# Optimization experiments

Measured on AMD Instinct MI355X. Metric: run time of the kernel, lower is better.

## Reference

```python
import jax, jax.numpy as jnp
import numpy as np

POS_DIM = 3
LATENT = 128
HEADS = 4
HEAD_DIM = LATENT // HEADS
KERNEL_IN = 4 * POS_DIM - POS_DIM + 1  # q_pos,o_pos,rel,dist -> 10
N_Q = 1024
N_O = 2048
LN_EPS = 1e-5


def setup_inputs() -> dict:
    key = jax.random.key(0)
    ks = jax.random.split(key, 9)
    s = lambda fan_in: 1.0 / np.sqrt(fan_in)
    return {
        "h_obs": jax.random.normal(ks[0], (N_O, LATENT), dtype=jnp.float32),
        "pos_obs": jax.random.normal(ks[1], (N_O, POS_DIM), dtype=jnp.float32),
        "pos_query": jax.random.normal(ks[2], (N_Q, POS_DIM), dtype=jnp.float32),
        "obs_batch": jnp.zeros((N_O,), dtype=jnp.int32),
        "query_batch": jnp.zeros((N_Q,), dtype=jnp.int32),
        # kernel_mlp: Linear(10, 128) -> ReLU -> Linear(128, 4); stored as [in, out]
        "W1": jax.random.uniform(ks[3], (KERNEL_IN, LATENT), jnp.float32, -s(KERNEL_IN), s(KERNEL_IN)),
        "b1": jnp.zeros((LATENT,), jnp.float32),
        "W2": jax.random.uniform(ks[4], (LATENT, HEADS), jnp.float32, -s(LATENT), s(LATENT)),
        "b2": jnp.zeros((HEADS,), jnp.float32),
        "ln_gamma": jnp.ones((LATENT,), jnp.float32),
        "ln_beta": jnp.zeros((LATENT,), jnp.float32),
        "Wv": jax.random.uniform(ks[5], (LATENT, LATENT), jnp.float32, -s(LATENT), s(LATENT)),
        "bv": jnp.zeros((LATENT,), jnp.float32),
    }


def reference(h_obs, pos_obs, pos_query, obs_batch, query_batch,
              W1, b1, W2, b2, ln_gamma, ln_beta, Wv, bv):
    N_q, N_o = pos_query.shape[0], pos_obs.shape[0]
    # pairwise relative position encodings: [N_q, N_o, 10]
    rel = pos_query[:, None, :] - pos_obs[None, :, :]            # [N_q, N_o, P]
    dist = jnp.linalg.norm(rel, axis=-1, keepdims=True)          # [N_q, N_o, 1]
    pos_q_exp = jnp.broadcast_to(pos_query[:, None, :], rel.shape)
    pos_o_exp = jnp.broadcast_to(pos_obs[None, :, :], rel.shape)
    kernel_input = jnp.concatenate([pos_q_exp, pos_o_exp, rel, dist], axis=-1)
    # per-pair MLP score -> logits [N_q, N_o, H]
    hidden = jax.nn.relu(jnp.einsum('qok,kl->qol', kernel_input, W1) + b1)
    logits = jnp.einsum('qol,lh->qoh', hidden, W2) + b2
    # same-graph mask (softmax over N_o axis)
    batch_mask = query_batch[:, None] == obs_batch[None, :]      # [N_q, N_o]
    logits = jnp.where(batch_mask[:, :, None], logits, -jnp.inf)
    weights = jax.nn.softmax(logits, axis=1)                     # over N_o
    # value path: LayerNorm -> value_proj -> heads
    mu = jnp.mean(h_obs, axis=-1, keepdims=True)
    var = jnp.var(h_obs, axis=-1, keepdims=True)
    h_norm = (h_obs - mu) * jax.lax.rsqrt(var + LN_EPS) * ln_gamma + ln_beta
    v = (h_norm @ Wv + bv).reshape(N_o, HEADS, HEAD_DIM)         # [N_o, H, D]
    # weighted aggregation: [N_q, H, D] -> [N_q, latent]
    h_query = jnp.einsum('qoh,ohd->qhd', weights, v)
    return h_query.reshape(N_q, LATENT)
```

## Files before the change

kernel.cpp:

```cpp
#include <hip/hip_runtime.h>

#define NQ 1024
#define NO 2048
#define LAT 128
#define CHUNK 16
#define NCHUNK (NO / CHUNK)
#define LDSTR 132
#define LOG2E 1.4426950408889634f
#define NEG_BIG -3.0e38f
#define MASK_THRESH -1.0e37f
#define PART_STRIDE 136
#define SY_MAX 32

__global__ __launch_bounds__(256) void gano_value(
    const float* __restrict__ ln_g,
    const float* __restrict__ ln_b,
    const float* __restrict__ Wv,
    const float* __restrict__ bv,
    float* __restrict__ h)
{
    __shared__ float hn[2][LAT];
    __shared__ float red[2][4];
    const int t = threadIdx.x;
    const int o = t >> 7;
    const int d = t & 127;
    const int ob = blockIdx.x * 2 + o;

    const float x = h[(size_t)ob*LAT + d];
    float s1 = x, s2 = x*x;
#pragma unroll
    for (int off = 32; off >= 1; off >>= 1) {
        s1 += __shfl_xor(s1, off);
        s2 += __shfl_xor(s2, off);
    }
    const int wv = (t >> 6) & 1;
    if ((t & 63) == 0) { red[o][wv*2] = s1; red[o][wv*2+1] = s2; }
    __syncthreads();
    const float S1 = red[o][0] + red[o][2];
    const float S2 = red[o][1] + red[o][3];
    const float mean = S1 * (1.0f/LAT);
    const float var  = S2 * (1.0f/LAT) - mean*mean;
    const float rstd = rsqrtf(var + 1e-5f);
    hn[o][d] = (x - mean) * rstd * ln_g[d] + ln_b[d];
    __syncthreads();

    float a0 = bv[d], a1 = 0.f, a2 = 0.f, a3 = 0.f;
    const float* wc = Wv + d;
    const float* hh = hn[o];
#pragma unroll 8
    for (int kk = 0; kk < 32; ++kk) {
        a0 = fmaf(hh[kk],      wc[(size_t)(kk)*LAT],      a0);
        a1 = fmaf(hh[kk + 32], wc[(size_t)(kk + 32)*LAT], a1);
        a2 = fmaf(hh[kk + 64], wc[(size_t)(kk + 64)*LAT], a2);
        a3 = fmaf(hh[kk + 96], wc[(size_t)(kk + 96)*LAT], a3);
    }
    h[(size_t)ob*LAT + d] = (a0 + a1) + (a2 + a3);
}

__global__ __launch_bounds__(256) void gano_main(
    const float* __restrict__ v,
    const float* __restrict__ pos_obs,
    const float* __restrict__ pos_query,
    const int* __restrict__ obs_batch,
    const int* __restrict__ query_batch,
    const float* __restrict__ W1,
    const float* __restrict__ b1,
    const float* __restrict__ W2,
    const float* __restrict__ b2,
    float* __restrict__ ws,
    float* __restrict__ out,
    int SY)
{
    __shared__ __align__(16) float ld[CHUNK*LDSTR];
    __shared__ __align__(16) float lcq[16*LDSTR];
    __shared__ __align__(16) float lgt[16*4*CHUNK];
    __shared__ float lpos[CHUNK*3];
    __shared__ int   lob[CHUNK];

    const int tid = threadIdx.x;
    const int i  = tid & 15;
    const int qi = tid >> 4;
    const int q  = blockIdx.x * 16 + qi;
    const int d0 = i * 8;
    const int hstar = i >> 2;

#pragma unroll
    for (int t2 = 0; t2 < 2; ++t2) {
        const int idx = tid + t2*256;
        const int row = idx >> 5;
        const int g   = idx & 31;
        const int dd4 = g * 4;
        const int qq  = blockIdx.x * 16 + row;
        const float px = pos_query[qq*3+0];
        const float py = pos_query[qq*3+1];
        const float pz = pos_query[qq*3+2];
        float4 c = *(const float4*)(b1 + dd4);
        const float4 wx0 = *(const float4*)(W1 + 0*LAT + dd4);
        const float4 wx6 = *(const float4*)(W1 + 6*LAT + dd4);
        const float4 wy0 = *(const float4*)(W1 + 1*LAT + dd4);
        const float4 wy6 = *(const float4*)(W1 + 7*LAT + dd4);
        const float4 wz0 = *(const float4*)(W1 + 2*LAT + dd4);
        const float4 wz6 = *(const float4*)(W1 + 8*LAT + dd4);
        c.x = fmaf(px, wx0.x+wx6.x, fmaf(py, wy0.x+wy6.x, fmaf(pz, wz0.x+wz6.x, c.x)));
        c.y = fmaf(px, wx0.y+wx6.y, fmaf(py, wy0.y+wy6.y, fmaf(pz, wz0.y+wz6.y, c.y)));
        c.z = fmaf(px, wx0.z+wx6.z, fmaf(py, wy0.z+wy6.z, fmaf(pz, wz0.z+wz6.z, c.z)));
        c.w = fmaf(px, wx0.w+wx6.w, fmaf(py, wy0.w+wy6.w, fmaf(pz, wz0.w+wz6.w, c.w)));
        *(float4*)(lcq + row*LDSTR + dd4) = c;
    }

    const float pqx = pos_query[q*3+0];
    const float pqy = pos_query[q*3+1];
    const float pqz = pos_query[q*3+2];
    const int   qb  = query_batch[q];
    const float b2l0 = b2[0]*LOG2E, b2l1 = b2[1]*LOG2E;
    const float b2l2 = b2[2]*LOG2E, b2l3 = b2[3]*LOG2E;

    float4 accA = make_float4(0.f,0.f,0.f,0.f);
    float4 accB = make_float4(0.f,0.f,0.f,0.f);
    float m = NEG_BIG, lsum = 0.f;

    for (int cb = blockIdx.y; cb < NCHUNK; cb += SY) {
        const int o0 = cb * CHUNK;
        __syncthreads();

#pragma unroll
        for (int t2 = 0; t2 < 2; ++t2) {
            const int idx = tid + t2*256;
            const int oo = idx >> 5;
            const int g  = idx & 31;
            const int d4 = g * 4;
            const float* po = pos_obs + (size_t)(o0 + oo)*3;
            const float px = po[0], py = po[1], pz = po[2];
            const float4 w3 = *(const float4*)(W1 + 3*LAT + d4);
            const float4 w4 = *(const float4*)(W1 + 4*LAT + d4);
            const float4 w5 = *(const float4*)(W1 + 5*LAT + d4);
            const float4 w6 = *(const float4*)(W1 + 6*LAT + d4);
            const float4 w7 = *(const float4*)(W1 + 7*LAT + d4);
            const float4 w8 = *(const float4*)(W1 + 8*LAT + d4);
            float4 r;
            r.x = fmaf(px, w3.x-w6.x, fmaf(py, w4.x-w7.x, pz*(w5.x-w8.x)));
            r.y = fmaf(px, w3.y-w6.y, fmaf(py, w4.y-w7.y, pz*(w5.y-w8.y)));
            r.z = fmaf(px, w3.z-w6.z, fmaf(py, w4.z-w7.z, pz*(w5.z-w8.z)));
            r.w = fmaf(px, w3.w-w6.w, fmaf(py, w4.w-w7.w, pz*(w5.w-w8.w)));
            *(float4*)(ld + oo*LDSTR + d4) = r;
        }
        for (int idx = tid; idx < CHUNK*3; idx += 256) lpos[idx] = pos_obs[o0*3 + idx];
        for (int idx = tid; idx < CHUNK;   idx += 256) lob[idx]  = obs_batch[o0 + idx];
        __syncthreads();

        {
            const int oc = i;
            const float dx = pqx - lpos[oc*3+0];
            const float dy = pqy - lpos[oc*3+1];
            const float dz = pqz - lpos[oc*3+2];
            const float dist = sqrtf(dx*dx + dy*dy + dz*dz);
            const int mb = (lob[oc] == qb);

            float lg0 = 0.f, lg1 = 0.f, lg2 = 0.f, lg3 = 0.f;
            const float* ldr = ld + oc*LDSTR;
            const float* lcr = lcq + qi*LDSTR;
#pragma unroll 4
            for (int j = 0; j < 32; ++j) {
                const float4 dd = *(const float4*)(ldr + j*4);
                const float4 cc = *(const float4*)(lcr + j*4);
                const float4 wd = *(const float4*)(W1 + 9*LAT + j*4);
                const float4 w2a = *(const float4*)(W2 + (j*4+0)*4);
                const float4 w2b = *(const float4*)(W2 + (j*4+1)*4);
                const float4 w2c = *(const float4*)(W2 + (j*4+2)*4);
                const float4 w2d = *(const float4*)(W2 + (j*4+3)*4);
                const float h0 = fmaxf(fmaf(wd.x, dist, cc.x + dd.x), 0.f);
                const float h1 = fmaxf(fmaf(wd.y, dist, cc.y + dd.y), 0.f);
                const float h2 = fmaxf(fmaf(wd.z, dist, cc.z + dd.z), 0.f);
                const float h3 = fmaxf(fmaf(wd.w, dist, cc.w + dd.w), 0.f);
                lg0 = fmaf(h0, w2a.x, lg0); lg1 = fmaf(h0, w2a.y, lg1);
                lg2 = fmaf(h0, w2a.z, lg2); lg3 = fmaf(h0, w2a.w, lg3);
                lg0 = fmaf(h1, w2b.x, lg0); lg1 = fmaf(h1, w2b.y, lg1);
                lg2 = fmaf(h1, w2b.z, lg2); lg3 = fmaf(h1, w2b.w, lg3);
                lg0 = fmaf(h2, w2c.x, lg0); lg1 = fmaf(h2, w2c.y, lg1);
                lg2 = fmaf(h2, w2c.z, lg2); lg3 = fmaf(h2, w2c.w, lg3);
                lg0 = fmaf(h3, w2d.x, lg0); lg1 = fmaf(h3, w2d.y, lg1);
                lg2 = fmaf(h3, w2d.z, lg2); lg3 = fmaf(h3, w2d.w, lg3);
            }
            const int ocr = (oc + 4*qi) & 15;
            float* lrow = lgt + (qi*4)*CHUNK + ocr;
            lrow[0*CHUNK] = mb ? fmaf(lg0, LOG2E, b2l0) : NEG_BIG;
            lrow[1*CHUNK] = mb ? fmaf(lg1, LOG2E, b2l1) : NEG_BIG;
            lrow[2*CHUNK] = mb ? fmaf(lg2, LOG2E, b2l2) : NEG_BIG;
            lrow[3*CHUNK] = mb ? fmaf(lg3, LOG2E, b2l3) : NEG_BIG;
        }
        __syncthreads();

        {
            const float* rowp = lgt + (qi*4 + hstar)*CHUNK;
#pragma unroll
            for (int og = 0; og < 4; ++og) {
                const float4 t4 = *(const float4*)(rowp + ((og + qi) & 3) * 4);
#pragma unroll
                for (int pr = 0; pr < 2; ++pr) {
                    const float l0 = pr ? t4.z : t4.x;
                    const float l1 = pr ? t4.w : t4.y;
                    const float mn = fmaxf(m, fmaxf(l0, l1));
                    const float alpha = exp2f(m - mn);
                    const float p0 = (l0 > MASK_THRESH) ? exp2f(l0 - mn) : 0.f;
                    const float p1 = (l1 > MASK_THRESH) ? exp2f(l1 - mn) : 0.f;
                    lsum = fmaf(lsum, alpha, p0 + p1);
                    m = mn;

                    const float* vp = v + (size_t)(o0 + og*4 + pr*2)*LAT + d0;
                    const float4 v0A = *(const float4*)(vp);
                    const float4 v0B = *(const float4*)(vp + 4);
                    const float4 v1A = *(const float4*)(vp + LAT);
                    const float4 v1B = *(const float4*)(vp + LAT + 4);
                    accA.x = fmaf(accA.x, alpha, fmaf(p0, v0A.x, p1*v1A.x));
                    accA.y = fmaf(accA.y, alpha, fmaf(p0, v0A.y, p1*v1A.y));
                    accA.z = fmaf(accA.z, alpha, fmaf(p0, v0A.z, p1*v1A.z));
                    accA.w = fmaf(accA.w, alpha, fmaf(p0, v0A.w, p1*v1A.w));
                    accB.x = fmaf(accB.x, alpha, fmaf(p0, v0B.x, p1*v1B.x));
                    accB.y = fmaf(accB.y, alpha, fmaf(p0, v0B.y, p1*v1B.y));
                    accB.z = fmaf(accB.z, alpha, fmaf(p0, v0B.z, p1*v1B.z));
                    accB.w = fmaf(accB.w, alpha, fmaf(p0, v0B.w, p1*v1B.w));
                }
            }
        }
    }

    if (SY == 1) {
        const float inv = 1.0f / lsum;
        float* op = out + (size_t)q*LAT + d0;
        float4 rA, rB;
        rA.x = accA.x*inv; rA.y = accA.y*inv; rA.z = accA.z*inv; rA.w = accA.w*inv;
        rB.x = accB.x*inv; rB.y = accB.y*inv; rB.z = accB.z*inv; rB.w = accB.w*inv;
        *(float4*)op       = rA;
        *(float4*)(op + 4) = rB;
    } else {
        float* pp = ws + ((size_t)blockIdx.y * NQ + q) * PART_STRIDE;
        if ((i & 3) == 0) {
            pp[hstar]     = m;
            pp[4 + hstar] = lsum;
        }
        *(float4*)(pp + 8 + d0)     = accA;
        *(float4*)(pp + 8 + d0 + 4) = accB;
    }
}

__global__ __launch_bounds__(128) void gano_combine(
    const float* __restrict__ ws, float* __restrict__ out, int SY)
{
    __shared__ float lm[SY_MAX*4];
    __shared__ float ll[SY_MAX*4];
    const int q = blockIdx.x;
    const int l = threadIdx.x;
    const int h = l >> 5;

    if (l < SY*4) {
        const int s = l >> 2, hh = l & 3;
        const float* pp = ws + ((size_t)s * NQ + q) * PART_STRIDE;
        lm[l] = pp[hh];
        ll[l] = pp[4 + hh];
    }
    __syncthreads();

    float M = NEG_BIG;
    for (int s = 0; s < SY; ++s) M = fmaxf(M, lm[s*4 + h]);

    float Ls = 0.f, A0 = 0.f, A1 = 0.f;
#pragma unroll 4
    for (int s = 0; s + 1 < SY; s += 2) {
        const float e0 = exp2f(lm[s*4 + h] - M);
        const float e1 = exp2f(lm[(s+1)*4 + h] - M);
        Ls = fmaf(ll[s*4 + h], e0, fmaf(ll[(s+1)*4 + h], e1, Ls));
        A0 = fmaf(ws[((size_t)s     * NQ + q) * PART_STRIDE + 8 + l], e0, A0);
        A1 = fmaf(ws[((size_t)(s+1) * NQ + q) * PART_STRIDE + 8 + l], e1, A1);
    }
    if (SY & 1) {
        const int s = SY - 1;
        const float e0 = exp2f(lm[s*4 + h] - M);
        Ls = fmaf(ll[s*4 + h], e0, Ls);
        A0 = fmaf(ws[((size_t)s * NQ + q) * PART_STRIDE + 8 + l], e0, A0);
    }
    out[(size_t)q*LAT + l] = (A0 + A1) / Ls;
}

extern "C" void kernel_launch(void* const* d_in, const int* in_sizes, int n_in,
                              void* d_out, int out_size, void* d_ws, size_t ws_size,
                              hipStream_t stream) {
    (void)in_sizes; (void)n_in; (void)out_size;
    float*       h_obs     = (float*)d_in[0];
    const float* pos_obs   = (const float*)d_in[1];
    const float* pos_query = (const float*)d_in[2];
    const int*   obs_batch = (const int*)d_in[3];
    const int*   query_batch = (const int*)d_in[4];
    const float* W1 = (const float*)d_in[5];
    const float* b1 = (const float*)d_in[6];
    const float* W2 = (const float*)d_in[7];
    const float* b2 = (const float*)d_in[8];
    const float* ln_g = (const float*)d_in[9];
    const float* ln_b = (const float*)d_in[10];
    const float* Wv = (const float*)d_in[11];
    const float* bv = (const float*)d_in[12];
    float* ws  = (float*)d_ws;
    float* out = (float*)d_out;

    int SY = 1;
    const size_t per = (size_t)NQ * PART_STRIDE * sizeof(float);
    if (ws && ws_size >= 2*per) {
        size_t s = ws_size / per;
        SY = (int)(s < SY_MAX ? s : SY_MAX);
    }

    gano_value<<<NO/2, 256, 0, stream>>>(ln_g, ln_b, Wv, bv, h_obs);
    gano_main<<<dim3(NQ/16, SY), 256, 0, stream>>>(h_obs, pos_obs, pos_query,
                                                   obs_batch, query_batch,
                                                   W1, b1, W2, b2, ws, out, SY);
    if (SY > 1)
        gano_combine<<<NQ, 128, 0, stream>>>(ws, out, SY);
}
```

Measured before the change: 191.6 us.

## Precompute per-observation W1 terms globally and fuse split-K combine via last-block atomic

Per-observation first-layer contributions are now computed once in the value kernel and stored in workspace, instead of being rebuilt into shared memory for every chunk by every query block. The main loop reads them from global memory, which removes the staging stores and one barrier per chunk. The separate combine kernel is removed: the last block for each query tile, found through an atomic counter, merges the partial softmax results. This saves a launch and a pass over the workspace, at the cost of extra global traffic in the inner loop and threadfence/atomic overhead.

```diff
diff --git a/kernel.cpp b/kernel.cpp
--- a/kernel.cpp
+++ b/kernel.cpp
@@ -12,12 +12,19 @@
 #define PART_STRIDE 136
 #define SY_MAX 32
 
+#define WS_DO   0
+#define WS_CNT  (NO*LAT)
+#define WS_PART (NO*LAT + 64)
+
 __global__ __launch_bounds__(256) void gano_value(
     const float* __restrict__ ln_g,
     const float* __restrict__ ln_b,
     const float* __restrict__ Wv,
     const float* __restrict__ bv,
-    float* __restrict__ h)
+    const float* __restrict__ W1,
+    const float* __restrict__ pos_obs,
+    float* __restrict__ h,
+    float* __restrict__ wsf)
 {
     __shared__ float hn[2][LAT];
     __shared__ float red[2][4];
@@ -35,6 +42,17 @@
     }
     const int wv = (t >> 6) & 1;
     if ((t & 63) == 0) { red[o][wv*2] = s1; red[o][wv*2+1] = s2; }
+
+    if (wsf) {
+        const float p0 = pos_obs[ob*3+0];
+        const float p1 = pos_obs[ob*3+1];
+        const float p2 = pos_obs[ob*3+2];
+        float ds =      p0 * (W1[3*LAT + d] - W1[6*LAT + d]);
+        ds = fmaf(p1,        W1[4*LAT + d] - W1[7*LAT + d], ds);
+        ds = fmaf(p2,        W1[5*LAT + d] - W1[8*LAT + d], ds);
+        wsf[WS_DO + (size_t)ob*LAT + d] = ds;
+        if (blockIdx.x == 0 && t < 64) ((int*)(wsf + WS_CNT))[t] = 0;
+    }
     __syncthreads();
     const float S1 = red[o][0] + red[o][2];
     const float S2 = red[o][1] + red[o][3];
@@ -71,11 +89,9 @@
     float* __restrict__ out,
     int SY)
 {
-    __shared__ __align__(16) float ld[CHUNK*LDSTR];
     __shared__ __align__(16) float lcq[16*LDSTR];
     __shared__ __align__(16) float lgt[16*4*CHUNK];
-    __shared__ float lpos[CHUNK*3];
-    __shared__ int   lob[CHUNK];
+    __shared__ int lastflag;
 
     const int tid = threadIdx.x;
     const int i  = tid & 15;
@@ -119,69 +135,83 @@
     float4 accB = make_float4(0.f,0.f,0.f,0.f);
     float m = NEG_BIG, lsum = 0.f;
 
+    const float* dob = ws ? (ws + WS_DO) : nullptr;
+
     for (int cb = blockIdx.y; cb < NCHUNK; cb += SY) {
         const int o0 = cb * CHUNK;
         __syncthreads();
 
-#pragma unroll
-        for (int t2 = 0; t2 < 2; ++t2) {
-            const int idx = tid + t2*256;
-            const int oo = idx >> 5;
-            const int g  = idx & 31;
-            const int d4 = g * 4;
-            const float* po = pos_obs + (size_t)(o0 + oo)*3;
-            const float px = po[0], py = po[1], pz = po[2];
-            const float4 w3 = *(const float4*)(W1 + 3*LAT + d4);
-            const float4 w4 = *(const float4*)(W1 + 4*LAT + d4);
-            const float4 w5 = *(const float4*)(W1 + 5*LAT + d4);
-            const float4 w6 = *(const float4*)(W1 + 6*LAT + d4);
-            const float4 w7 = *(const float4*)(W1 + 7*LAT + d4);
-            const float4 w8 = *(const float4*)(W1 + 8*LAT + d4);
-            float4 r;
-            r.x = fmaf(px, w3.x-w6.x, fmaf(py, w4.x-w7.x, pz*(w5.x-w8.x)));
-            r.y = fmaf(px, w3.y-w6.y, fmaf(py, w4.y-w7.y, pz*(w5.y-w8.y)));
-            r.z = fmaf(px, w3.z-w6.z, fmaf(py, w4.z-w7.z, pz*(w5.z-w8.z)));
-            r.w = fmaf(px, w3.w-w6.w, fmaf(py, w4.w-w7.w, pz*(w5.w-w8.w)));
-            *(float4*)(ld + oo*LDSTR + d4) = r;
-        }
-        for (int idx = tid; idx < CHUNK*3; idx += 256) lpos[idx] = pos_obs[o0*3 + idx];
-        for (int idx = tid; idx < CHUNK;   idx += 256) lob[idx]  = obs_batch[o0 + idx];
-        __syncthreads();
-
         {
-            const int oc = i;
-            const float dx = pqx - lpos[oc*3+0];
-            const float dy = pqy - lpos[oc*3+1];
-            const float dz = pqz - lpos[oc*3+2];
+            const int obs = o0 + i;
+            const float px = pos_obs[obs*3+0];
+            const float py = pos_obs[obs*3+1];
+            const float pz = pos_obs[obs*3+2];
+            const float dx = pqx - px, dy = pqy - py, dz = pqz - pz;
             const float dist = sqrtf(dx*dx + dy*dy + dz*dz);
-            const int mb = (lob[oc] == qb);
+            const int mb = (obs_batch[obs] == qb);
 
             float lg0 = 0.f, lg1 = 0.f, lg2 = 0.f, lg3 = 0.f;
-            const float* ldr = ld + oc*LDSTR;
             const float* lcr = lcq + qi*LDSTR;
+            if (dob) {
+                const float* dr = dob + (size_t)obs*LAT;
 #pragma unroll 4
-            for (int j = 0; j < 32; ++j) {
-                const float4 dd = *(const float4*)(ldr + j*4);
-                const float4 cc = *(const float4*)(lcr + j*4);
-                const float4 wd = *(const float4*)(W1 + 9*LAT + j*4);
-                const float4 w2a = *(const float4*)(W2 + (j*4+0)*4);
-                const float4 w2b = *(const float4*)(W2 + (j*4+1)*4);
-                const float4 w2c = *(const float4*)(W2 + (j*4+2)*4);
-                const float4 w2d = *(const float4*)(W2 + (j*4+3)*4);
-                const float h0 = fmaxf(fmaf(wd.x, dist, cc.x + dd.x), 0.f);
-                const float h1 = fmaxf(fmaf(wd.y, dist, cc.y + dd.y), 0.f);
-                const float h2 = fmaxf(fmaf(wd.z, dist, cc.z + dd.z), 0.f);
-                const float h3 = fmaxf(fmaf(wd.w, dist, cc.w + dd.w), 0.f);
-                lg0 = fmaf(h0, w2a.x, lg0); lg1 = fmaf(h0, w2a.y, lg1);
-                lg2 = fmaf(h0, w2a.z, lg2); lg3 = fmaf(h0, w2a.w, lg3);
-                lg0 = fmaf(h1, w2b.x, lg0); lg1 = fmaf(h1, w2b.y, lg1);
-                lg2 = fmaf(h1, w2b.z, lg2); lg3 = fmaf(h1, w2b.w, lg3);
-                lg0 = fmaf(h2, w2c.x, lg0); lg1 = fmaf(h2, w2c.y, lg1);
-                lg2 = fmaf(h2, w2c.z, lg2); lg3 = fmaf(h2, w2c.w, lg3);
-                lg0 = fmaf(h3, w2d.x, lg0); lg1 = fmaf(h3, w2d.y, lg1);
-                lg2 = fmaf(h3, w2d.z, lg2); lg3 = fmaf(h3, w2d.w, lg3);
+                for (int j = 0; j < 32; ++j) {
+                    const float4 dd = *(const float4*)(dr + j*4);
+                    const float4 cc = *(const float4*)(lcr + j*4);
+                    const float4 wd = *(const float4*)(W1 + 9*LAT + j*4);
+                    const float4 w2a = *(const float4*)(W2 + (j*4+0)*4);
+                    const float4 w2b = *(const float4*)(W2 + (j*4+1)*4);
+                    const float4 w2c = *(const float4*)(W2 + (j*4+2)*4);
+                    const float4 w2d = *(const float4*)(W2 + (j*4+3)*4);
+                    const float h0 = fmaxf(fmaf(wd.x, dist, cc.x + dd.x), 0.f);
+                    const float h1 = fmaxf(fmaf(wd.y, dist, cc.y + dd.y), 0.f);
+                    const float h2 = fmaxf(fmaf(wd.z, dist, cc.z + dd.z), 0.f);
+                    const float h3 = fmaxf(fmaf(wd.w, dist, cc.w + dd.w), 0.f);
+                    lg0 = fmaf(h0, w2a.x, lg0); lg1 = fmaf(h0, w2a.y, lg1);
+                    lg2 = fmaf(h0, w2a.z, lg2); lg3 = fmaf(h0, w2a.w, lg3);
+                    lg0 = fmaf(h1, w2b.x, lg0); lg1 = fmaf(h1, w2b.y, lg1);
+                    lg2 = fmaf(h1, w2b.z, lg2); lg3 = fmaf(h1, w2b.w, lg3);
+                    lg0 = fmaf(h2, w2c.x, lg0); lg1 = fmaf(h2, w2c.y, lg1);
+                    lg2 = fmaf(h2, w2c.z, lg2); lg3 = fmaf(h2, w2c.w, lg3);
+                    lg0 = fmaf(h3, w2d.x, lg0); lg1 = fmaf(h3, w2d.y, lg1);
+                    lg2 = fmaf(h3, w2d.z, lg2); lg3 = fmaf(h3, w2d.w, lg3);
+                }
+            } else {
+#pragma unroll 2
+                for (int j = 0; j < 32; ++j) {
+                    const int d4 = j*4;
+                    const float4 w3 = *(const float4*)(W1 + 3*LAT + d4);
+                    const float4 w4 = *(const float4*)(W1 + 4*LAT + d4);
+                    const float4 w5 = *(const float4*)(W1 + 5*LAT + d4);
+                    const float4 w6 = *(const float4*)(W1 + 6*LAT + d4);
+                    const float4 w7 = *(const float4*)(W1 + 7*LAT + d4);
+                    const float4 w8 = *(const float4*)(W1 + 8*LAT + d4);
+                    float4 dd;
+                    dd.x = fmaf(px, w3.x-w6.x, fmaf(py, w4.x-w7.x, pz*(w5.x-w8.x)));
+                    dd.y = fmaf(px, w3.y-w6.y, fmaf(py, w4.y-w7.y, pz*(w5.y-w8.y)));
+                    dd.z = fmaf(px, w3.z-w6.z, fmaf(py, w4.z-w7.z, pz*(w5.z-w8.z)));
+                    dd.w = fmaf(px, w3.w-w6.w, fmaf(py, w4.w-w7.w, pz*(w5.w-w8.w)));
+                    const float4 cc = *(const float4*)(lcr + d4);
+                    const float4 wd = *(const float4*)(W1 + 9*LAT + d4);
+                    const float4 w2a = *(const float4*)(W2 + (d4+0)*4);
+                    const float4 w2b = *(const float4*)(W2 + (d4+1)*4);
+                    const float4 w2c = *(const float4*)(W2 + (d4+2)*4);
+                    const float4 w2d = *(const float4*)(W2 + (d4+3)*4);
+                    const float h0 = fmaxf(fmaf(wd.x, dist, cc.x + dd.x), 0.f);
+                    const float h1 = fmaxf(fmaf(wd.y, dist, cc.y + dd.y), 0.f);
+                    const float h2 = fmaxf(fmaf(wd.z, dist, cc.z + dd.z), 0.f);
+                    const float h3 = fmaxf(fmaf(wd.w, dist, cc.w + dd.w), 0.f);
+                    lg0 = fmaf(h0, w2a.x, lg0); lg1 = fmaf(h0, w2a.y, lg1);
+                    lg2 = fmaf(h0, w2a.z, lg2); lg3 = fmaf(h0, w2a.w, lg3);
+                    lg0 = fmaf(h1, w2b.x, lg0); lg1 = fmaf(h1, w2b.y, lg1);
+                    lg2 = fmaf(h1, w2b.z, lg2); lg3 = fmaf(h1, w2b.w, lg3);
+                    lg0 = fmaf(h2, w2c.x, lg0); lg1 = fmaf(h2, w2c.y, lg1);
+                    lg2 = fmaf(h2, w2c.z, lg2); lg3 = fmaf(h2, w2c.w, lg3);
+                    lg0 = fmaf(h3, w2d.x, lg0); lg1 = fmaf(h3, w2d.y, lg1);
+                    lg2 = fmaf(h3, w2d.z, lg2); lg3 = fmaf(h3, w2d.w, lg3);
+                }
             }
-            const int ocr = (oc + 4*qi) & 15;
+            const int ocr = (i + 4*qi) & 15;
             float* lrow = lgt + (qi*4)*CHUNK + ocr;
             lrow[0*CHUNK] = mb ? fmaf(lg0, LOG2E, b2l0) : NEG_BIG;
             lrow[1*CHUNK] = mb ? fmaf(lg1, LOG2E, b2l1) : NEG_BIG;
@@ -232,8 +262,11 @@
         rB.x = accB.x*inv; rB.y = accB.y*inv; rB.z = accB.z*inv; rB.w = accB.w*inv;
         *(float4*)op       = rA;
         *(float4*)(op + 4) = rB;
-    } else {
-        float* pp = ws + ((size_t)blockIdx.y * NQ + q) * PART_STRIDE;
+        return;
+    }
+
+    {
+        float* pp = ws + WS_PART + ((size_t)blockIdx.y * NQ + q) * PART_STRIDE;
         if ((i & 3) == 0) {
             pp[hstar]     = m;
             pp[4 + hstar] = lsum;
@@ -241,44 +274,41 @@
         *(float4*)(pp + 8 + d0)     = accA;
         *(float4*)(pp + 8 + d0 + 4) = accB;
     }
-}
-
-__global__ __launch_bounds__(128) void gano_combine(
-    const float* __restrict__ ws, float* __restrict__ out, int SY)
-{
-    __shared__ float lm[SY_MAX*4];
-    __shared__ float ll[SY_MAX*4];
-    const int q = blockIdx.x;
-    const int l = threadIdx.x;
-    const int h = l >> 5;
-
-    if (l < SY*4) {
-        const int s = l >> 2, hh = l & 3;
-        const float* pp = ws + ((size_t)s * NQ + q) * PART_STRIDE;
-        lm[l] = pp[hh];
-        ll[l] = pp[4 + hh];
-    }
     __syncthreads();
-
-    float M = NEG_BIG;
-    for (int s = 0; s < SY; ++s) M = fmaxf(M, lm[s*4 + h]);
-
-    float Ls = 0.f, A0 = 0.f, A1 = 0.f;
-#pragma unroll 4
-    for (int s = 0; s + 1 < SY; s += 2) {
-        const float e0 = exp2f(lm[s*4 + h] - M);
-        const float e1 = exp2f(lm[(s+1)*4 + h] - M);
-        Ls = fmaf(ll[s*4 + h], e0, fmaf(ll[(s+1)*4 + h], e1, Ls));
-        A0 = fmaf(ws[((size_t)s     * NQ + q) * PART_STRIDE + 8 + l], e0, A0);
-        A1 = fmaf(ws[((size_t)(s+1) * NQ + q) * PART_STRIDE + 8 + l], e1, A1);
-    }
-    if (SY & 1) {
-        const int s = SY - 1;
-        const float e0 = exp2f(lm[s*4 + h] - M);
-        Ls = fmaf(ll[s*4 + h], e0, Ls);
-        A0 = fmaf(ws[((size_t)s * NQ + q) * PART_STRIDE + 8 + l], e0, A0);
-    }
-    out[(size_t)q*LAT + l] = (A0 + A1) / Ls;
+    if (tid == 0) {
+        __threadfence();
+        int* cnt = (int*)(ws + WS_CNT);
+        lastflag = (atomicAdd(&cnt[blockIdx.x], 1) == SY - 1);
+    }
+    __syncthreads();
+    if (lastflag) {
+        __threadfence();
+        const float* base = ws + WS_PART;
+        float M = NEG_BIG;
+        for (int s = 0; s < SY; ++s)
+            M = fmaxf(M, base[((size_t)s * NQ + q) * PART_STRIDE + hstar]);
+        float Ls = 0.f;
+        float4 A0 = make_float4(0.f,0.f,0.f,0.f);
+        float4 A1 = make_float4(0.f,0.f,0.f,0.f);
+        for (int s = 0; s < SY; ++s) {
+            const float* pp = base + ((size_t)s * NQ + q) * PART_STRIDE;
+            const float e = exp2f(pp[hstar] - M);
+            Ls = fmaf(pp[4 + hstar], e, Ls);
+            const float4 xa = *(const float4*)(pp + 8 + d0);
+            const float4 xb = *(const float4*)(pp + 8 + d0 + 4);
+            A0.x = fmaf(e, xa.x, A0.x); A0.y = fmaf(e, xa.y, A0.y);
+            A0.z = fmaf(e, xa.z, A0.z); A0.w = fmaf(e, xa.w, A0.w);
+            A1.x = fmaf(e, xb.x, A1.x); A1.y = fmaf(e, xb.y, A1.y);
+            A1.z = fmaf(e, xb.z, A1.z); A1.w = fmaf(e, xb.w, A1.w);
+        }
+        const float inv = 1.0f / Ls;
+        float* op = out + (size_t)q*LAT + d0;
+        float4 rA, rB;
+        rA.x = A0.x*inv; rA.y = A0.y*inv; rA.z = A0.z*inv; rA.w = A0.w*inv;
+        rB.x = A1.x*inv; rB.y = A1.y*inv; rB.z = A1.z*inv; rB.w = A1.w*inv;
+        *(float4*)op       = rA;
+        *(float4*)(op + 4) = rB;
+    }
 }
 
 extern "C" void kernel_launch(void* const* d_in, const int* in_sizes, int n_in,
@@ -301,17 +331,19 @@
     float* ws  = (float*)d_ws;
     float* out = (float*)d_out;
 
+    const size_t fixed = (size_t)WS_PART * sizeof(float);
+    const size_t per   = (size_t)NQ * PART_STRIDE * sizeof(float);
     int SY = 1;
-    const size_t per = (size_t)NQ * PART_STRIDE * sizeof(float);
-    if (ws && ws_size >= 2*per) {
-        size_t s = ws_size / per;
+    float* wsf = nullptr;
+    if (ws && ws_size >= fixed + 2*per) {
+        size_t s = (ws_size - fixed) / per;
         SY = (int)(s < SY_MAX ? s : SY_MAX);
-    }
-
-    gano_value<<<NO/2, 256, 0, stream>>>(ln_g, ln_b, Wv, bv, h_obs);
+        wsf = ws;
+    }
+
+    gano_value<<<NO/2, 256, 0, stream>>>(ln_g, ln_b, Wv, bv, W1, pos_obs,
+                                         h_obs, wsf);
     gano_main<<<dim3(NQ/16, SY), 256, 0, stream>>>(h_obs, pos_obs, pos_query,
                                                    obs_batch, query_batch,
-                                                   W1, b1, W2, b2, ws, out, SY);
-    if (SY > 1)
-        gano_combine<<<NQ, 128, 0, stream>>>(ws, out, SY);
+                                                   W1, b1, W2, b2, wsf, out, SY);
 }
```

After: 313.7 us. 63.8% more time.
